# Kernel optimization log

Hardware: AMD Instinct MI355X
Metric: run time of the kernel (lower is better)

Reference implementation:

```python
import jax, jax.numpy as jnp
import numpy as np

N, E, B = 20000, 160000, 1024
MDIM, EDIM, H, L, PROP = 64, 16, 128, 4, 1000


def _lin(key, fan_in, fan_out, scale=None):
    s = scale if scale is not None else 1.0 / np.sqrt(fan_in)
    return (jax.random.normal(key, (fan_in, fan_out), jnp.float32) * s)


def setup_inputs() -> dict:
    key = jax.random.key(0)
    ks = iter(jax.random.split(key, 64))
    d = {}
    d["x"] = jax.random.normal(next(ks), (N, MDIM), jnp.float32)
    d["pos"] = jax.random.normal(next(ks), (N, 3), jnp.float32)
    d["edge_attr"] = jax.random.normal(next(ks), (E, EDIM), jnp.float32)
    d["edge_index"] = jax.random.randint(next(ks), (2, E), 0, N)
    d["batch"] = jnp.sort(jax.random.randint(next(ks), (N,), 0, B))
    # EGNN embeddings
    d["emb_in_w"] = _lin(next(ks), MDIM, H); d["emb_in_b"] = jnp.zeros((H,), jnp.float32)
    d["emb_out_w"] = _lin(next(ks), H, H); d["emb_out_b"] = jnp.zeros((H,), jnp.float32)
    # per-layer E_GCL params, stacked over layers
    ein = 2 * H + 1 + EDIM  # [h_row, h_col, radial, edge_attr]
    d["edge_w1"] = jnp.stack([_lin(next(ks), ein, H) for _ in range(L)]); d["edge_b1"] = jnp.zeros((L, H), jnp.float32)
    d["edge_w2"] = jnp.stack([_lin(next(ks), H, H) for _ in range(L)]); d["edge_b2"] = jnp.zeros((L, H), jnp.float32)
    d["node_w1"] = jnp.stack([_lin(next(ks), 2 * H, H) for _ in range(L)]); d["node_b1"] = jnp.zeros((L, H), jnp.float32)
    d["node_w2"] = jnp.stack([_lin(next(ks), H, H) for _ in range(L)]); d["node_b2"] = jnp.zeros((L, H), jnp.float32)
    d["coord_w1"] = jnp.stack([_lin(next(ks), H, H) for _ in range(L)]); d["coord_b1"] = jnp.zeros((L, H), jnp.float32)
    d["coord_w2"] = jnp.stack([_lin(next(ks), H, 1, scale=0.001) for _ in range(L)])  # xavier gain=0.001, no bias
    # end_layers: 2 ResBlocks (Dropout->Linear->SiLU->Linear) + head
    d["res_w1"] = jnp.stack([_lin(next(ks), H, H) for _ in range(2)]); d["res_b1"] = jnp.zeros((2, H), jnp.float32)
    d["res_w2"] = jnp.stack([_lin(next(ks), H, H) for _ in range(2)]); d["res_b2"] = jnp.zeros((2, H), jnp.float32)
    d["head_w"] = _lin(next(ks), H, PROP); d["head_b"] = jnp.zeros((PROP,), jnp.float32)
    return d


def _egnn_forward(x, pos, edge_attr, edge_index, batch,
                  emb_in_w, emb_in_b, emb_out_w, emb_out_b,
                  edge_w1, edge_b1, edge_w2, edge_b2,
                  node_w1, node_b1, node_w2, node_b2,
                  coord_w1, coord_b1, coord_w2,
                  res_w1, res_b1, res_w2, res_b2, head_w, head_b):
    silu = jax.nn.silu
    row, col = edge_index[0], edge_index[1]
    h = x @ emb_in_w + emb_in_b                                   # [N, H]
    # edge in-degree counts for coords_agg='mean' (clamped to >=1)
    cnt = jax.ops.segment_sum(jnp.ones((E, 1), h.dtype), row, num_segments=N)
    cnt = jnp.maximum(cnt, 1.0)
    for l in range(L):
        coord_diff = pos[row] - pos[col]                          # [E, 3]
        radial = jnp.sum(coord_diff * coord_diff, axis=-1, keepdims=True)  # [E, 1]
        # edge model
        e_in = jnp.concatenate([h[row], h[col], radial, edge_attr], axis=-1)
        m = silu(silu(e_in @ edge_w1[l] + edge_b1[l]) @ edge_w2[l] + edge_b2[l])  # [E, H]
        # coord model (coords_agg='mean')
        trans = coord_diff * (silu(m @ coord_w1[l] + coord_b1[l]) @ coord_w2[l])  # [E, 3]
        pos = pos + jax.ops.segment_sum(trans, row, num_segments=N) / cnt
        # node model (residual=True)
        agg = jax.ops.segment_sum(m, row, num_segments=N)         # [N, H]
        n_in = jnp.concatenate([h, agg], axis=-1)
        h = h + (silu(n_in @ node_w1[l] + node_b1[l]) @ node_w2[l] + node_b2[l])
    h = h @ emb_out_w + emb_out_b
    g = jax.ops.segment_max(h, batch, num_segments=B)             # [B, H]
    for r in range(2):
        g = g + (silu(g @ res_w1[r] + res_b1[r]) @ res_w2[r] + res_b2[r])
    return g @ head_w + head_b                                    # [B, PROP]


def reference(x, pos, edge_attr, edge_index, batch,
              emb_in_w, emb_in_b, emb_out_w, emb_out_b,
              edge_w1, edge_b1, edge_w2, edge_b2,
              node_w1, node_b1, node_w2, node_b2,
              coord_w1, coord_b1, coord_w2,
              res_w1, res_b1, res_w2, res_b2, head_w, head_b):
    return _egnn_forward(x, pos, edge_attr, edge_index, batch,
                         emb_in_w, emb_in_b, emb_out_w, emb_out_b,
                         edge_w1, edge_b1, edge_w2, edge_b2,
                         node_w1, node_b1, node_w2, node_b2,
                         coord_w1, coord_b1, coord_w2,
                         res_w1, res_b1, res_w2, res_b2, head_w, head_b)
```

## Files before the change

kernel.cpp:

```cpp
#include <hip/hip_runtime.h>
#include <hip/hip_bf16.h>

#define HD 128
#define PROP 1000
#define NPB  8

typedef float f32x4 __attribute__((ext_vector_type(4)));
typedef short s16x8 __attribute__((ext_vector_type(8)));

__device__ __forceinline__ float silu_f(float v) { return v / (1.0f + __expf(-v)); }

__device__ __forceinline__ unsigned short f2bf(float f) {
    union { __hip_bfloat16 h; unsigned short u; } v;
    v.h = __float2bfloat16(f);
    return v.u;
}
__device__ __forceinline__ unsigned pk2(float a, float b) {
    union { __hip_bfloat162 h; unsigned u; } v;
    v.h = __float22bfloat162_rn(make_float2(a, b));
    return v.u;
}
__device__ __forceinline__ float bf2f_lo(unsigned u) { return __uint_as_float(u << 16); }
__device__ __forceinline__ float bf2f_hi(unsigned u) { return __uint_as_float(u & 0xffff0000u); }
__device__ __forceinline__ float4 ld4(const float* p) { return *(const float4*)p; }
__device__ __forceinline__ unsigned enc_max(float f) {
    unsigned u = __float_as_uint(f);
    return (u & 0x80000000u) ? ~u : (u | 0x80000000u);
}


__global__ void counti_kernel(const int* __restrict__ ei, int* __restrict__ cnt, int E) {
    int e = blockIdx.x * 256 + threadIdx.x;
    if (e < E) atomicAdd(&cnt[ei[e]], 1);
}

__global__ __launch_bounds__(1024) void scan_blk(
    const int* __restrict__ cnt, int* __restrict__ excl, int* __restrict__ bsum, int N)
{
    __shared__ int wsum[16], wexc[17];
    const int t = threadIdx.x, lane = t & 63, wid = t >> 6;
    const int gid = blockIdx.x * 1024 + t;
    int v = (gid < N) ? cnt[gid] : 0;
    int incl = v;
    #pragma unroll
    for (int d = 1; d < 64; d <<= 1) {
        int x = __shfl_up(incl, d, 64);
        if (lane >= d) incl += x;
    }
    if (lane == 63) wsum[wid] = incl;
    __syncthreads();
    if (t == 0) {
        int a = 0;
        #pragma unroll
        for (int w2 = 0; w2 < 16; ++w2) { wexc[w2] = a; a += wsum[w2]; }
        wexc[16] = a;
    }
    __syncthreads();
    if (gid < N) excl[gid] = wexc[wid] + incl - v;
    if (t == 0) bsum[blockIdx.x] = wexc[16];
}
__global__ __launch_bounds__(64) void scan_top(int* __restrict__ bsum, int nb) {
    const int lane = threadIdx.x;
    int v = (lane < nb) ? bsum[lane] : 0;
    int incl = v;
    #pragma unroll
    for (int d = 1; d < 64; d <<= 1) {
        int x = __shfl_up(incl, d, 64);
        if (lane >= d) incl += x;
    }
    if (lane < nb) bsum[lane] = incl - v;
}
__global__ void scan_add(const int* __restrict__ excl, const int* __restrict__ bsum,
                         int* __restrict__ rp, int* __restrict__ wp, int N, int E) {
    int gid = blockIdx.x * 256 + threadIdx.x;
    if (gid < N) {
        int r = excl[gid] + bsum[gid >> 10];
        rp[gid] = r; wp[gid] = r;
    }
    if (gid == 0) rp[N] = E;
}

__global__ void scatter_kernel(const int* __restrict__ ei, int* __restrict__ wp,
                               int* __restrict__ perm, int* __restrict__ rows_s,
                               int* __restrict__ cols_s, int E) {
    int e = blockIdx.x * 256 + threadIdx.x;
    if (e < E) {
        int r = ei[e];
        int p = atomicAdd(&wp[r], 1);
        perm[p] = e;
        rows_s[p] = r;
        cols_s[p] = ei[E + e];
    }
}

__global__ void eattr_perm_kernel(const float* __restrict__ eattr, const int* __restrict__ perm,
                                  unsigned short* __restrict__ eperm, int E) {
    int i = blockIdx.x * 256 + threadIdx.x;
    if (i >= E) return;
    const float* src = eattr + (size_t)perm[i] * 16;
    float4 a = ld4(src), b = ld4(src + 4), c = ld4(src + 8), d = ld4(src + 12);
    unsigned short* dst = eperm + (size_t)i * 16;
    *(uint4*)dst       = make_uint4(pk2(a.x, a.y), pk2(a.z, a.w), pk2(b.x, b.y), pk2(b.z, b.w));
    *(uint4*)(dst + 8) = make_uint4(pk2(c.x, c.y), pk2(c.z, c.w), pk2(d.x, d.y), pk2(d.z, d.w));
}

__global__ void prep_w1nc(const float* __restrict__ ew1, unsigned short* __restrict__ dst) {
    int idx = blockIdx.x * 256 + threadIdx.x;
    if (idx >= 4 * 256 * 128) return;
    int k = idx & 127, o2 = (idx >> 7) & 255, l = idx >> 15;
    dst[idx] = f2bf(ew1[((size_t)l * 273 + k + ((o2 >> 7) << 7)) * 128 + (o2 & 127)]);
}
__global__ void prep_wattr(const float* __restrict__ ew1, unsigned short* __restrict__ dst) {
    int idx = blockIdx.x * 256 + threadIdx.x;
    if (idx >= 4 * 128 * 32) return;
    int k = idx & 31, o = (idx >> 5) & 127, l = idx >> 12;
    int ksrc = (k < 16) ? (257 + k) : (k == 16 ? 256 : -1);
    float v = (ksrc >= 0) ? ew1[((size_t)l * 273 + ksrc) * 128 + o] : 0.0f;
    dst[idx] = f2bf(v);
}
__global__ void prep_t(const float* __restrict__ src, unsigned short* __restrict__ dst, int K) {
    int idx = blockIdx.x * 256 + threadIdx.x;
    if (idx >= 4 * 128 * K) return;
    int k = idx % K, o = (idx / K) & 127, l = idx / (K * 128);
    dst[idx] = f2bf(src[((size_t)l * K + k) * 128 + o]);
}
__global__ void prep_t1(const float* __restrict__ src, unsigned short* __restrict__ dst) {
    int idx = blockIdx.x * 256 + threadIdx.x;
    if (idx >= 128 * 128) return;
    int k = idx & 127, o = idx >> 7;
    dst[idx] = f2bf(src[(size_t)k * 128 + o]);
}
__global__ void prep_t_sig(const float* __restrict__ src, unsigned short* __restrict__ dst) {
    int idx = blockIdx.x * 256 + threadIdx.x;
    if (idx >= 4 * 128 * 128) return;
    int k = idx & 127, o = (idx >> 7) & 127, l = idx >> 14;
    int ks = ((k >> 2) & 7) * 16 + ((k >> 5) << 2) + (k & 3);
    dst[idx] = f2bf(src[((size_t)l * 128 + ks) * 128 + o]);
}
__global__ void prep_wemb(const float* __restrict__ src, unsigned short* __restrict__ dst) {
    int idx = blockIdx.x * 256 + threadIdx.x;
    if (idx >= 128 * 64) return;
    int k = idx & 63, o = idx >> 6;
    dst[idx] = f2bf(src[(size_t)k * 128 + o]);
}

__global__ __launch_bounds__(128) void emb_pre_kernel(
    const float* __restrict__ x, const unsigned short* __restrict__ wembt,
    const float* __restrict__ bemb,
    const unsigned short* __restrict__ w1nc, const float* __restrict__ b1,
    float* __restrict__ h, unsigned short* __restrict__ apre, int N)
{
    __shared__ __align__(16) char s_xt[32 * 128];
    __shared__ __align__(16) char s_h[32 * 256];
    const int tid = threadIdx.x;
    const int lane = tid & 63, wid = tid >> 6;
    const int lr = lane & 15, kg = lane >> 4;
    const int n0 = blockIdx.x * 32 + wid * 16;
    {
        int n16 = lane >> 2, q = lane & 3;
        int nn = min(n0 + n16, N - 1);
        int sw2 = (n16 & 7) << 4;
        char* row = s_xt + (wid * 16 + n16) * 128;
        #pragma unroll
        for (int it = 0; it < 4; ++it) {
            float4 v = ld4(x + (size_t)nn * 64 + q * 16 + it * 4);
            *(uint2*)(row + ((q * 32 + it * 8) ^ sw2)) = make_uint2(pk2(v.x, v.y), pk2(v.z, v.w));
        }
    }
    const int nd = n0 + lr;
    const int sw = (lr & 7) << 4;
    f32x4 acc[8];
    #pragma unroll
    for (int mf = 0; mf < 8; ++mf) acc[mf] = (f32x4){0.f, 0.f, 0.f, 0.f};
    {
        const char* brow = s_xt + (wid * 16 + lr) * 128;
        for (int ks = 0; ks < 2; ++ks) {
            s16x8 b = *(const s16x8*)(brow + ((ks * 64 + kg * 16) ^ sw));
            #pragma unroll
            for (int mf = 0; mf < 8; ++mf) {
                s16x8 a = *(const s16x8*)(wembt + (size_t)(mf * 16 + lr) * 64 + ks * 32 + kg * 8);
                acc[mf] = __builtin_amdgcn_mfma_f32_16x16x32_bf16(a, b, acc[mf], 0, 0, 0);
            }
        }
    }
    char* hrow = s_h + (wid * 16 + lr) * 256;
    #pragma unroll
    for (int mf = 0; mf < 8; ++mf) {
        f32x4 bb = *(const f32x4*)(bemb + mf * 16 + kg * 4);
        float v0 = acc[mf][0] + bb[0];
        float v1 = acc[mf][1] + bb[1];
        float v2 = acc[mf][2] + bb[2];
        float v3 = acc[mf][3] + bb[3];
        if (nd < N) *(f32x4*)(h + (size_t)nd * HD + mf * 16 + kg * 4) = (f32x4){v0, v1, v2, v3};
        *(uint2*)(hrow + ((mf * 32 + kg * 8) ^ sw)) = make_uint2(pk2(v0, v1), pk2(v2, v3));
    }
    f32x4 acc2[16];
    #pragma unroll
    for (int mf = 0; mf < 16; ++mf) acc2[mf] = (f32x4){0.f, 0.f, 0.f, 0.f};
    for (int ks = 0; ks < 4; ++ks) {
        s16x8 b = *(const s16x8*)(hrow + ((ks * 64 + kg * 16) ^ sw));
        #pragma unroll
        for (int mf = 0; mf < 16; ++mf) {
            s16x8 a = *(const s16x8*)(w1nc + (size_t)(mf * 16 + lr) * 128 + ks * 32 + kg * 8);
            acc2[mf] = __builtin_amdgcn_mfma_f32_16x16x32_bf16(a, b, acc2[mf], 0, 0, 0);
        }
    }
    if (nd < N) {
        #pragma unroll
        for (int mf = 0; mf < 16; ++mf) {
            float b0 = 0.f, b1v = 0.f, b2v = 0.f, b3v = 0.f;
            if (mf < 8) {
                f32x4 bb = *(const f32x4*)(b1 + mf * 16 + kg * 4);
                b0 = bb[0]; b1v = bb[1]; b2v = bb[2]; b3v = bb[3];
            }
            int pos = ((mf >> 3) << 7) + kg * 32 + (mf & 7) * 4;
            *(uint2*)(apre + (size_t)nd * 256 + pos) =
                make_uint2(pk2(acc2[mf][0] + b0, acc2[mf][1] + b1v), pk2(acc2[mf][2] + b2v, acc2[mf][3] + b3v));
        }
    }
}

__global__ __launch_bounds__(64) void edge_compute_kernel(
    const float* __restrict__ pos, const unsigned short* __restrict__ apre,
    const unsigned short* __restrict__ eperm,
    const int* __restrict__ rows_s, const int* __restrict__ cols_s,
    const unsigned short* __restrict__ wattr,
    const unsigned short* __restrict__ wt2, const float* __restrict__ b2,
    const unsigned short* __restrict__ cwt1, const float* __restrict__ cb1,
    const float* __restrict__ cw2,
    unsigned short* __restrict__ medge, float* __restrict__ trans, int E)
{
    __shared__ __align__(16) char s_m[16 * 256];
    __shared__ __align__(16) char s_g[16 * 256];

    int wg = blockIdx.x;
    {
        int nper = gridDim.x >> 3;
        if ((gridDim.x & 7) == 0) wg = (wg & 7) * nper + (wg >> 3);
    }
    const int lane = threadIdx.x;
    const int lr = lane & 15, kg = lane >> 4;
    const int i0 = wg * 16;
    const int i = i0 + lr;
    const bool valid = i < E;
    const int ic = min(i, E - 1);
    const int r = rows_s[ic], c = cols_s[ic];

    {
        int e = lane >> 2, q = lane & 3;
        int ce = cols_s[min(i0 + e, E - 1)];
        const char* src = (const char*)(apre + (size_t)ce * 256 + 128);
        char* dst = s_g + e * 256;
        int sw2 = (e & 7) << 4;
        #pragma unroll
        for (int it = 0; it < 4; ++it) {
            uint4 v = *(const uint4*)(src + it * 64 + q * 16);
            *(uint4*)(dst + ((it * 64 + q * 16) ^ sw2)) = v;
        }
    }

    float dx = pos[r*3+0] - pos[c*3+0];
    float dy = pos[r*3+1] - pos[c*3+1];
    float dz = pos[r*3+2] - pos[c*3+2];
    float rad = dx*dx + dy*dy + dz*dz;

    union { s16x8 v; unsigned u[4]; } battr;
    if (kg < 2) {
        battr.v = *(const s16x8*)(eperm + (size_t)ic * 16 + kg * 8);
    } else {
        battr.u[0] = (kg == 2) ? pk2(rad, 0.f) : 0u;
        battr.u[1] = 0u; battr.u[2] = 0u; battr.u[3] = 0u;
    }

    uint4 rgq[4];
    {
        const unsigned short* rb = apre + (size_t)r * 256 + kg * 32;
        #pragma unroll
        for (int q = 0; q < 4; ++q) rgq[q] = *(const uint4*)(rb + q * 8);
    }
    uint4 cgq[4];
    {
        const char* g = s_g + lr * 256;
        int swl = (lr & 7) << 4;
        #pragma unroll
        for (int q = 0; q < 4; ++q)
            cgq[q] = *(const uint4*)(g + ((kg * 64 + q * 16) ^ swl));
    }

    char* mrow = s_m + lr * 256;
    const int sw = (lr & 7) << 4;

    f32x4 acc[8];
    #pragma unroll
    for (int mf = 0; mf < 8; ++mf) acc[mf] = (f32x4){0.f, 0.f, 0.f, 0.f};
    #pragma unroll
    for (int mf = 0; mf < 8; ++mf) {
        s16x8 a = *(const s16x8*)(wattr + (size_t)(mf * 16 + lr) * 32 + kg * 8);
        acc[mf] = __builtin_amdgcn_mfma_f32_16x16x32_bf16(a, battr.v, acc[mf], 0, 0, 0);
    }
    #pragma unroll
    for (int mf = 0; mf < 8; ++mf) {
        unsigned rlo = ((const unsigned*)&rgq[mf >> 1])[(mf & 1) * 2];
        unsigned rhi = ((const unsigned*)&rgq[mf >> 1])[(mf & 1) * 2 + 1];
        unsigned clo = ((const unsigned*)&cgq[mf >> 1])[(mf & 1) * 2];
        unsigned chi = ((const unsigned*)&cgq[mf >> 1])[(mf & 1) * 2 + 1];
        float v0 = silu_f(acc[mf][0] + bf2f_lo(rlo) + bf2f_lo(clo));
        float v1 = silu_f(acc[mf][1] + bf2f_hi(rlo) + bf2f_hi(clo));
        float v2 = silu_f(acc[mf][2] + bf2f_lo(rhi) + bf2f_lo(chi));
        float v3 = silu_f(acc[mf][3] + bf2f_hi(rhi) + bf2f_hi(chi));
        *(uint2*)(mrow + ((kg * 64 + mf * 8) ^ sw)) = make_uint2(pk2(v0, v1), pk2(v2, v3));
    }

    #pragma unroll
    for (int mf = 0; mf < 8; ++mf) acc[mf] = (f32x4){0.f, 0.f, 0.f, 0.f};
    for (int ks = 0; ks < 4; ++ks) {
        s16x8 b = *(const s16x8*)(mrow + ((ks * 64 + kg * 16) ^ sw));
        #pragma unroll
        for (int mf = 0; mf < 8; ++mf) {
            s16x8 a = *(const s16x8*)(wt2 + (size_t)(mf * 16 + lr) * 128 + ks * 32 + kg * 8);
            acc[mf] = __builtin_amdgcn_mfma_f32_16x16x32_bf16(a, b, acc[mf], 0, 0, 0);
        }
    }
    #pragma unroll
    for (int mf = 0; mf < 8; ++mf) {
        f32x4 bb = *(const f32x4*)(b2 + mf * 16 + kg * 4);
        float v0 = silu_f(acc[mf][0] + bb[0]);
        float v1 = silu_f(acc[mf][1] + bb[1]);
        float v2 = silu_f(acc[mf][2] + bb[2]);
        float v3 = silu_f(acc[mf][3] + bb[3]);
        *(uint2*)(mrow + ((mf * 32 + kg * 8) ^ sw)) = make_uint2(pk2(v0, v1), pk2(v2, v3));
    }

    #pragma unroll
    for (int mf = 0; mf < 8; ++mf) acc[mf] = (f32x4){0.f, 0.f, 0.f, 0.f};
    for (int ks = 0; ks < 4; ++ks) {
        s16x8 b = *(const s16x8*)(mrow + ((ks * 64 + kg * 16) ^ sw));
        #pragma unroll
        for (int mf = 0; mf < 8; ++mf) {
            s16x8 a = *(const s16x8*)(cwt1 + (size_t)(mf * 16 + lr) * 128 + ks * 32 + kg * 8);
            acc[mf] = __builtin_amdgcn_mfma_f32_16x16x32_bf16(a, b, acc[mf], 0, 0, 0);
        }
    }

    {
        int e = lane >> 2, q = lane & 3;
        int ie = i0 + e;
        if (ie < E) {
            const char* src = s_m + e * 256;
            int sw2 = (e & 7) << 4;
            char* dst = (char*)(medge + (size_t)ie * HD);
            #pragma unroll
            for (int it = 0; it < 4; ++it) {
                uint4 v = *(const uint4*)(src + ((it * 64 + q * 16) ^ sw2));
                *(uint4*)(dst + it * 64 + q * 16) = v;
            }
        }
    }

    float part = 0.f;
    #pragma unroll
    for (int mf = 0; mf < 8; ++mf) {
        f32x4 bb = *(const f32x4*)(cb1 + mf * 16 + kg * 4);
        f32x4 cw = *(const f32x4*)(cw2 + mf * 16 + kg * 4);
        part += silu_f(acc[mf][0] + bb[0]) * cw[0];
        part += silu_f(acc[mf][1] + bb[1]) * cw[1];
        part += silu_f(acc[mf][2] + bb[2]) * cw[2];
        part += silu_f(acc[mf][3] + bb[3]) * cw[3];
    }
    part += __shfl_xor(part, 16, 64);
    part += __shfl_xor(part, 32, 64);
    if (valid && kg == 0)
        *(float4*)(trans + (size_t)i * 4) = make_float4(dx * part, dy * part, dz * part, 0.f);
}

__global__ __launch_bounds__(64) void node_fused_kernel(
    float* __restrict__ h, const unsigned short* __restrict__ medge,
    const float* __restrict__ trans, const int* __restrict__ rp,
    float* __restrict__ pos,
    const unsigned short* __restrict__ nw1t, const float* __restrict__ nb1,
    const unsigned short* __restrict__ nw2t, const float* __restrict__ nb2,
    const unsigned short* __restrict__ w1nc_next, const float* __restrict__ b1_next,
    unsigned short* __restrict__ apre, int N, int has_next)
{
    __shared__ __align__(16) char s_x[16 * 512];
    const int lane = threadIdx.x;
    const int lr = lane & 15, kg = lane >> 4;
    const int n0 = blockIdx.x * 16;
    {
        int n16 = lane >> 2, q = lane & 3;
        int nn = min(n0 + n16, N - 1);
        int sw2 = (n16 & 7) << 4;
        char* row = s_x + n16 * 512;
        #pragma unroll
        for (int it = 0; it < 8; ++it) {
            int c2 = q * 32 + it * 4;
            float4 v = ld4(h + (size_t)nn * HD + c2);
            *(uint2*)(row + ((c2 * 2) ^ sw2)) = make_uint2(pk2(v.x, v.y), pk2(v.z, v.w));
        }
        const int s = rp[nn], e2 = rp[nn + 1];
        float a[32];
        #pragma unroll
        for (int t = 0; t < 32; ++t) a[t] = 0.f;
        for (int j = s; j < e2; ++j) {
            const unsigned short* mp = medge + (size_t)j * HD + q * 32;
            #pragma unroll
            for (int v4 = 0; v4 < 4; ++v4) {
                uint4 w = *(const uint4*)(mp + v4 * 8);
                a[v4*8+0] += bf2f_lo(w.x); a[v4*8+1] += bf2f_hi(w.x);
                a[v4*8+2] += bf2f_lo(w.y); a[v4*8+3] += bf2f_hi(w.y);
                a[v4*8+4] += bf2f_lo(w.z); a[v4*8+5] += bf2f_hi(w.z);
                a[v4*8+6] += bf2f_lo(w.w); a[v4*8+7] += bf2f_hi(w.w);
            }
        }
        #pragma unroll
        for (int it2 = 0; it2 < 4; ++it2) {
            uint4 w = make_uint4(pk2(a[it2*8+0], a[it2*8+1]), pk2(a[it2*8+2], a[it2*8+3]),
                                 pk2(a[it2*8+4], a[it2*8+5]), pk2(a[it2*8+6], a[it2*8+7]));
            *(uint4*)(row + ((256 + q * 64 + it2 * 16) ^ sw2)) = w;
        }
        if (q < 3 && n0 + n16 < N) {
            float pa = 0.f;
            for (int j = s; j < e2; ++j) pa += trans[(size_t)j * 4 + q];
            pos[(size_t)(n0 + n16) * 3 + q] += pa / fmaxf((float)(e2 - s), 1.0f);
        }
    }
    const int nd = n0 + lr;
    char* brow = s_x + lr * 512;
    const int sw = (lr & 7) << 4;
    f32x4 acc[8];
    #pragma unroll
    for (int mf = 0; mf < 8; ++mf) acc[mf] = (f32x4){0.f, 0.f, 0.f, 0.f};
    for (int ks = 0; ks < 8; ++ks) {
        s16x8 b = *(const s16x8*)(brow + ((ks * 64 + kg * 16) ^ sw));
        #pragma unroll
        for (int mf = 0; mf < 8; ++mf) {
            s16x8 a = *(const s16x8*)(nw1t + (size_t)(mf * 16 + lr) * 256 + ks * 32 + kg * 8);
            acc[mf] = __builtin_amdgcn_mfma_f32_16x16x32_bf16(a, b, acc[mf], 0, 0, 0);
        }
    }
    #pragma unroll
    for (int mf = 0; mf < 8; ++mf) {
        f32x4 bb = *(const f32x4*)(nb1 + mf * 16 + kg * 4);
        float v0 = silu_f(acc[mf][0] + bb[0]);
        float v1 = silu_f(acc[mf][1] + bb[1]);
        float v2 = silu_f(acc[mf][2] + bb[2]);
        float v3 = silu_f(acc[mf][3] + bb[3]);
        *(uint2*)(brow + ((mf * 32 + kg * 8) ^ sw)) = make_uint2(pk2(v0, v1), pk2(v2, v3));
    }
    #pragma unroll
    for (int mf = 0; mf < 8; ++mf) acc[mf] = (f32x4){0.f, 0.f, 0.f, 0.f};
    for (int ks = 0; ks < 4; ++ks) {
        s16x8 b = *(const s16x8*)(brow + ((ks * 64 + kg * 16) ^ sw));
        #pragma unroll
        for (int mf = 0; mf < 8; ++mf) {
            s16x8 a = *(const s16x8*)(nw2t + (size_t)(mf * 16 + lr) * 128 + ks * 32 + kg * 8);
            acc[mf] = __builtin_amdgcn_mfma_f32_16x16x32_bf16(a, b, acc[mf], 0, 0, 0);
        }
    }
    uint2 hpk[8];
    if (nd < N) {
        #pragma unroll
        for (int mf = 0; mf < 8; ++mf) {
            f32x4 bb = *(const f32x4*)(nb2 + mf * 16 + kg * 4);
            float* hp = h + (size_t)nd * HD + mf * 16 + kg * 4;
            f32x4 hv = *(const f32x4*)hp;
            hv[0] += acc[mf][0] + bb[0];
            hv[1] += acc[mf][1] + bb[1];
            hv[2] += acc[mf][2] + bb[2];
            hv[3] += acc[mf][3] + bb[3];
            *(f32x4*)hp = hv;
            hpk[mf] = make_uint2(pk2(hv[0], hv[1]), pk2(hv[2], hv[3]));
        }
    }
    if (!has_next) return;
    #pragma unroll
    for (int mf = 0; mf < 8; ++mf)
        *(uint2*)(brow + ((mf * 32 + kg * 8) ^ sw)) = hpk[mf];
    f32x4 acc2[16];
    #pragma unroll
    for (int mf = 0; mf < 16; ++mf) acc2[mf] = (f32x4){0.f, 0.f, 0.f, 0.f};
    for (int ks = 0; ks < 4; ++ks) {
        s16x8 b = *(const s16x8*)(brow + ((ks * 64 + kg * 16) ^ sw));
        #pragma unroll
        for (int mf = 0; mf < 16; ++mf) {
            s16x8 a = *(const s16x8*)(w1nc_next + (size_t)(mf * 16 + lr) * 128 + ks * 32 + kg * 8);
            acc2[mf] = __builtin_amdgcn_mfma_f32_16x16x32_bf16(a, b, acc2[mf], 0, 0, 0);
        }
    }
    if (nd < N) {
        #pragma unroll
        for (int mf = 0; mf < 16; ++mf) {
            float b0 = 0.f, b1v = 0.f, b2v = 0.f, b3v = 0.f;
            if (mf < 8) {
                f32x4 bb = *(const f32x4*)(b1_next + mf * 16 + kg * 4);
                b0 = bb[0]; b1v = bb[1]; b2v = bb[2]; b3v = bb[3];
            }
            int pos2 = ((mf >> 3) << 7) + kg * 32 + (mf & 7) * 4;
            *(uint2*)(apre + (size_t)nd * 256 + pos2) =
                make_uint2(pk2(acc2[mf][0] + b0, acc2[mf][1] + b1v), pk2(acc2[mf][2] + b2v, acc2[mf][3] + b3v));
        }
    }
}

__global__ void ginit_kernel(unsigned* __restrict__ g_enc, int n) {
    int i = blockIdx.x * 256 + threadIdx.x;
    if (i < n) g_enc[i] = 0x007FFFFFu;
}

__global__ __launch_bounds__(64) void embout_mfma_kernel(
    const float* __restrict__ h, const unsigned short* __restrict__ wot,
    const float* __restrict__ b, const int* __restrict__ batch,
    unsigned* __restrict__ g_enc, int N)
{
    __shared__ __align__(16) char s_h[16 * 256];
    __shared__ __align__(16) float s_out[16 * 128];
    const int lane = threadIdx.x;
    const int lr = lane & 15, kg = lane >> 4;
    const int n0 = blockIdx.x * 16;
    {
        int n16 = lane >> 2, q = lane & 3;
        int nn = min(n0 + n16, N - 1);
        int sw2 = (n16 & 7) << 4;
        char* row = s_h + n16 * 256;
        #pragma unroll
        for (int it = 0; it < 8; ++it) {
            int c2 = q * 32 + it * 4;
            float4 v = ld4(h + (size_t)nn * HD + c2);
            *(uint2*)(row + ((c2 * 2) ^ sw2)) = make_uint2(pk2(v.x, v.y), pk2(v.z, v.w));
        }
    }
    const char* brow = s_h + lr * 256;
    const int sw = (lr & 7) << 4;
    f32x4 acc[8];
    #pragma unroll
    for (int mf = 0; mf < 8; ++mf) acc[mf] = (f32x4){0.f, 0.f, 0.f, 0.f};
    for (int ks = 0; ks < 4; ++ks) {
        s16x8 bv = *(const s16x8*)(brow + ((ks * 64 + kg * 16) ^ sw));
        #pragma unroll
        for (int mf = 0; mf < 8; ++mf) {
            s16x8 a = *(const s16x8*)(wot + (size_t)(mf * 16 + lr) * 128 + ks * 32 + kg * 8);
            acc[mf] = __builtin_amdgcn_mfma_f32_16x16x32_bf16(a, bv, acc[mf], 0, 0, 0);
        }
    }
    #pragma unroll
    for (int mf = 0; mf < 8; ++mf) {
        f32x4 bb = *(const f32x4*)(b + mf * 16 + kg * 4);
        f32x4 v = { acc[mf][0] + bb[0], acc[mf][1] + bb[1], acc[mf][2] + bb[2], acc[mf][3] + bb[3] };
        *(f32x4*)(s_out + lr * 128 + mf * 16 + kg * 4) = v;
    }
    const int nmax = min(16, N - n0);
    float m0 = -3.4e38f, m1 = -3.4e38f;
    int cur = batch[n0];
    for (int e = 0; e < nmax; ++e) {
        int bi = batch[n0 + e];
        if (bi != cur) {
            atomicMax(&g_enc[(size_t)cur * HD + lane], enc_max(m0));
            atomicMax(&g_enc[(size_t)cur * HD + 64 + lane], enc_max(m1));
            m0 = -3.4e38f; m1 = -3.4e38f; cur = bi;
        }
        m0 = fmaxf(m0, s_out[e * 128 + lane]);
        m1 = fmaxf(m1, s_out[e * 128 + 64 + lane]);
    }
    atomicMax(&g_enc[(size_t)cur * HD + lane], enc_max(m0));
    atomicMax(&g_enc[(size_t)cur * HD + 64 + lane], enc_max(m1));
}

__global__ __launch_bounds__(128) void resblock_kernel(
    const unsigned* __restrict__ g_enc,
    const float* __restrict__ rw1, const float* __restrict__ rb1,
    const float* __restrict__ rw2, const float* __restrict__ rb2,
    float* __restrict__ g)
{
    __shared__ float s_g[HD];
    __shared__ float s_t[HD];
    const int b = blockIdx.x, j = threadIdx.x;
    unsigned u = g_enc[(size_t)b * HD + j];
    float v = (u & 0x80000000u) ? __uint_as_float(u & 0x7FFFFFFFu) : __uint_as_float(~u);
    s_g[j] = v;
    __syncthreads();
    for (int r = 0; r < 2; ++r) {
        float a1 = rb1[r * HD + j];
        for (int k = 0; k < HD; ++k) a1 += s_g[k] * rw1[(size_t)r * HD * HD + (size_t)k * HD + j];
        s_t[j] = silu_f(a1);
        __syncthreads();
        float a2 = rb2[r * HD + j];
        for (int k = 0; k < HD; ++k) a2 += s_t[k] * rw2[(size_t)r * HD * HD + (size_t)k * HD + j];
        __syncthreads();
        s_g[j] += a2;
        __syncthreads();
    }
    g[(size_t)b * HD + j] = s_g[j];
}

__global__ __launch_bounds__(256) void head_kernel(
    const float* __restrict__ g, const float* __restrict__ hw, const float* __restrict__ hb,
    float* __restrict__ out, int B)
{
    __shared__ __align__(16) float s_g[HD][8];
    const int b0 = blockIdx.y * 8;
    const int p = blockIdx.x * 256 + threadIdx.x;
    for (int t = threadIdx.x; t < 8 * HD; t += 256) {
        int b = t & 7, k = t >> 3;
        s_g[k][b] = g[(size_t)min(b0 + b, B - 1) * HD + k];
    }
    __syncthreads();
    if (p >= PROP) return;
    float hbp = hb[p];
    float acc[8];
    #pragma unroll
    for (int b = 0; b < 8; ++b) acc[b] = hbp;
    for (int k = 0; k < HD; ++k) {
        float w = hw[(size_t)k * PROP + p];
        float4 g0 = *(const float4*)&s_g[k][0];
        float4 g1 = *(const float4*)&s_g[k][4];
        acc[0] += g0.x * w; acc[1] += g0.y * w; acc[2] += g0.z * w; acc[3] += g0.w * w;
        acc[4] += g1.x * w; acc[5] += g1.y * w; acc[6] += g1.z * w; acc[7] += g1.w * w;
    }
    #pragma unroll
    for (int b = 0; b < 8; ++b)
        if (b0 + b < B) out[(size_t)(b0 + b) * PROP + p] = acc[b];
}

extern "C" void kernel_launch(void* const* d_in, const int* in_sizes, int n_in,
                              void* d_out, int out_size, void* d_ws, size_t ws_size,
                              hipStream_t stream)
{
    const float* x        = (const float*)d_in[0];
    const float* pos_in   = (const float*)d_in[1];
    const float* eattr    = (const float*)d_in[2];
    const int*   ei       = (const int*)d_in[3];
    const int*   batch    = (const int*)d_in[4];
    const float* emb_in_w = (const float*)d_in[5];
    const float* emb_in_b = (const float*)d_in[6];
    const float* emb_out_w= (const float*)d_in[7];
    const float* emb_out_b= (const float*)d_in[8];
    const float* ew1 = (const float*)d_in[9];
    const float* eb1 = (const float*)d_in[10];
    const float* ew2 = (const float*)d_in[11];
    const float* eb2 = (const float*)d_in[12];
    const float* nw1 = (const float*)d_in[13];
    const float* nb1 = (const float*)d_in[14];
    const float* nw2 = (const float*)d_in[15];
    const float* nb2 = (const float*)d_in[16];
    const float* cw1 = (const float*)d_in[17];
    const float* cb1 = (const float*)d_in[18];
    const float* cw2 = (const float*)d_in[19];
    const float* rw1 = (const float*)d_in[20];
    const float* rb1 = (const float*)d_in[21];
    const float* rw2 = (const float*)d_in[22];
    const float* rb2 = (const float*)d_in[23];
    const float* hw  = (const float*)d_in[24];
    const float* hb  = (const float*)d_in[25];
    float* out = (float*)d_out;
    (void)ws_size;

    const int N = in_sizes[0] / 64;
    const int E = in_sizes[2] / 16;
    const int B = out_size / PROP;

    float* wsf = (float*)d_ws;
    float* pos_cur = wsf;   wsf += (size_t)N * 3;
    float* h       = wsf;   wsf += (size_t)N * HD;
    float* g       = wsf;   wsf += (size_t)B * HD;
    float* trans   = wsf;   wsf += (size_t)E * 4;
    wsf += (4 - (((size_t)(wsf - (float*)d_ws)) & 3)) & 3;
    unsigned short* apre  = (unsigned short*)wsf;
    unsigned short* eperm = apre  + (size_t)N * 256;
    unsigned short* w1nc  = eperm + (size_t)E * 16;
    unsigned short* wattr = w1nc  + (size_t)4 * 256 * 128;
    unsigned short* wt2   = wattr + (size_t)4 * 128 * 32;
    unsigned short* cwt1  = wt2   + (size_t)4 * 128 * 128;
    unsigned short* nw1t  = cwt1  + (size_t)4 * 128 * 128;
    unsigned short* nw2t  = nw1t  + (size_t)4 * 128 * 256;
    unsigned short* wembt = nw2t  + (size_t)4 * 128 * 128;
    unsigned short* wot   = wembt + (size_t)128 * 64;
    unsigned short* medge = wot   + (size_t)128 * 128;
    int* ip   = (int*)(medge + (size_t)E * HD);
    unsigned* g_enc = (unsigned*)ip;  ip += (size_t)B * HD;
    int* cnt_i = ip;  ip += N;
    int* rp    = ip;  ip += N + 1;
    int* wp    = ip;  ip += N;
    int* excl  = ip;  ip += N;
    int* bsum  = ip;  ip += 64;
    int* perm  = ip;  ip += E;
    int* rows_s= ip;  ip += E;
    int* cols_s= ip;  ip += E;

    prep_w1nc<<<(4 * 256 * 128 + 255) / 256, 256, 0, stream>>>(ew1, w1nc);
    prep_wattr<<<(4 * 128 * 32 + 255) / 256, 256, 0, stream>>>(ew1, wattr);
    prep_t_sig<<<(4 * 128 * 128 + 255) / 256, 256, 0, stream>>>(ew2, wt2);
    prep_t<<<(4 * 128 * 128 + 255) / 256, 256, 0, stream>>>(cw1, cwt1, 128);
    prep_t<<<(4 * 128 * 256 + 255) / 256, 256, 0, stream>>>(nw1, nw1t, 256);
    prep_t<<<(4 * 128 * 128 + 255) / 256, 256, 0, stream>>>(nw2, nw2t, 128);
    prep_wemb<<<(128 * 64 + 255) / 256, 256, 0, stream>>>(emb_in_w, wembt);
    prep_t1<<<(128 * 128 + 255) / 256, 256, 0, stream>>>(emb_out_w, wot);

    hipMemsetAsync(cnt_i, 0, (size_t)N * sizeof(int), stream);
    counti_kernel<<<(E + 255) / 256, 256, 0, stream>>>(ei, cnt_i, E);
    const int nb = (N + 1023) / 1024;
    scan_blk<<<nb, 1024, 0, stream>>>(cnt_i, excl, bsum, N);
    scan_top<<<1, 64, 0, stream>>>(bsum, nb);
    scan_add<<<(N + 255) / 256, 256, 0, stream>>>(excl, bsum, rp, wp, N, E);
    scatter_kernel<<<(E + 255) / 256, 256, 0, stream>>>(ei, wp, perm, rows_s, cols_s, E);
    eattr_perm_kernel<<<(E + 255) / 256, 256, 0, stream>>>(eattr, perm, eperm, E);

    hipMemcpyAsync(pos_cur, pos_in, (size_t)N * 3 * sizeof(float),
                   hipMemcpyDeviceToDevice, stream);

    emb_pre_kernel<<<(N + 31) / 32, 128, 0, stream>>>(x, wembt, emb_in_b, w1nc, eb1, h, apre, N);
    const int nblk = (N + 15) / 16;
    for (int l = 0; l < 4; ++l) {
        edge_compute_kernel<<<(E + 15) / 16, 64, 0, stream>>>(
            pos_cur, apre, eperm, rows_s, cols_s,
            wattr + (size_t)l * 128 * 32,
            wt2  + (size_t)l * 128 * 128, eb2 + (size_t)l * HD,
            cwt1 + (size_t)l * 128 * 128, cb1 + (size_t)l * HD,
            cw2 + (size_t)l * HD,
            medge, trans, E);
        node_fused_kernel<<<nblk, 64, 0, stream>>>(
            h, medge, trans, rp, pos_cur,
            nw1t + (size_t)l * 128 * 256, nb1 + (size_t)l * HD,
            nw2t + (size_t)l * 128 * 128, nb2 + (size_t)l * HD,
            w1nc + (size_t)(l + 1 < 4 ? l + 1 : 0) * 256 * 128,
            eb1 + (size_t)(l + 1 < 4 ? l + 1 : 0) * HD,
            apre, N, l < 3 ? 1 : 0);
    }

    ginit_kernel<<<(B * HD + 255) / 256, 256, 0, stream>>>(g_enc, B * HD);
    embout_mfma_kernel<<<nblk, 64, 0, stream>>>(h, wot, emb_out_b, batch, g_enc, N);
    resblock_kernel<<<B, 128, 0, stream>>>(g_enc, rw1, rb1, rw2, rb2, g);
    head_kernel<<<dim3((PROP + 255) / 256, (B + 7) / 8), 256, 0, stream>>>(g, hw, hb, out, B);
}
```

Measured before the change: 662.7 us.

## Process two 16-edge tiles per wave in edge kernel and merge prep launches

The edge compute kernel now handles 32 edges per 64-thread workgroup as two 16-edge tiles. Each weight fragment loaded from global memory feeds two MFMAs, one per tile, which halves weight-load traffic per edge and gives the scheduler more independent work. In exchange the kernel uses twice the accumulator registers and LDS, which may lower occupancy. Separately, the eight weight-prep kernels and the g_enc init kernel are folded into one prep_all launch to cut launch overhead.

```diff
diff --git a/kernel.cpp b/kernel.cpp
--- a/kernel.cpp
+++ b/kernel.cpp
@@ -104,44 +104,69 @@
     *(uint4*)(dst + 8) = make_uint4(pk2(c.x, c.y), pk2(c.z, c.w), pk2(d.x, d.y), pk2(d.z, d.w));
 }
 
-__global__ void prep_w1nc(const float* __restrict__ ew1, unsigned short* __restrict__ dst) {
+__global__ void prep_all(
+    const float* __restrict__ ew1, const float* __restrict__ ew2, const float* __restrict__ cw1,
+    const float* __restrict__ nw1, const float* __restrict__ nw2,
+    const float* __restrict__ emb_in_w, const float* __restrict__ emb_out_w,
+    unsigned short* __restrict__ w1nc, unsigned short* __restrict__ wattr,
+    unsigned short* __restrict__ wt2, unsigned short* __restrict__ cwt1,
+    unsigned short* __restrict__ nw1t, unsigned short* __restrict__ nw2t,
+    unsigned short* __restrict__ wembt, unsigned short* __restrict__ wot,
+    unsigned* __restrict__ g_enc, int ng)
+{
     int idx = blockIdx.x * 256 + threadIdx.x;
-    if (idx >= 4 * 256 * 128) return;
-    int k = idx & 127, o2 = (idx >> 7) & 255, l = idx >> 15;
-    dst[idx] = f2bf(ew1[((size_t)l * 273 + k + ((o2 >> 7) << 7)) * 128 + (o2 & 127)]);
-}
-__global__ void prep_wattr(const float* __restrict__ ew1, unsigned short* __restrict__ dst) {
-    int idx = blockIdx.x * 256 + threadIdx.x;
-    if (idx >= 4 * 128 * 32) return;
-    int k = idx & 31, o = (idx >> 5) & 127, l = idx >> 12;
-    int ksrc = (k < 16) ? (257 + k) : (k == 16 ? 256 : -1);
-    float v = (ksrc >= 0) ? ew1[((size_t)l * 273 + ksrc) * 128 + o] : 0.0f;
-    dst[idx] = f2bf(v);
-}
-__global__ void prep_t(const float* __restrict__ src, unsigned short* __restrict__ dst, int K) {
-    int idx = blockIdx.x * 256 + threadIdx.x;
-    if (idx >= 4 * 128 * K) return;
-    int k = idx % K, o = (idx / K) & 127, l = idx / (K * 128);
-    dst[idx] = f2bf(src[((size_t)l * K + k) * 128 + o]);
-}
-__global__ void prep_t1(const float* __restrict__ src, unsigned short* __restrict__ dst) {
-    int idx = blockIdx.x * 256 + threadIdx.x;
-    if (idx >= 128 * 128) return;
-    int k = idx & 127, o = idx >> 7;
-    dst[idx] = f2bf(src[(size_t)k * 128 + o]);
-}
-__global__ void prep_t_sig(const float* __restrict__ src, unsigned short* __restrict__ dst) {
-    int idx = blockIdx.x * 256 + threadIdx.x;
-    if (idx >= 4 * 128 * 128) return;
-    int k = idx & 127, o = (idx >> 7) & 127, l = idx >> 14;
-    int ks = ((k >> 2) & 7) * 16 + ((k >> 5) << 2) + (k & 3);
-    dst[idx] = f2bf(src[((size_t)l * 128 + ks) * 128 + o]);
-}
-__global__ void prep_wemb(const float* __restrict__ src, unsigned short* __restrict__ dst) {
-    int idx = blockIdx.x * 256 + threadIdx.x;
-    if (idx >= 128 * 64) return;
-    int k = idx & 63, o = idx >> 6;
-    dst[idx] = f2bf(src[(size_t)k * 128 + o]);
+    if (idx < 131072) {
+        int k = idx & 127, o2 = (idx >> 7) & 255, l = idx >> 15;
+        w1nc[idx] = f2bf(ew1[((size_t)l * 273 + k + ((o2 >> 7) << 7)) * 128 + (o2 & 127)]);
+        return;
+    }
+    idx -= 131072;
+    if (idx < 16384) {
+        int k = idx & 31, o = (idx >> 5) & 127, l = idx >> 12;
+        int ksrc = (k < 16) ? (257 + k) : (k == 16 ? 256 : -1);
+        float v = (ksrc >= 0) ? ew1[((size_t)l * 273 + ksrc) * 128 + o] : 0.0f;
+        wattr[idx] = f2bf(v);
+        return;
+    }
+    idx -= 16384;
+    if (idx < 65536) {
+        int k = idx & 127, o = (idx >> 7) & 127, l = idx >> 14;
+        int ks = ((k >> 2) & 7) * 16 + ((k >> 5) << 2) + (k & 3);
+        wt2[idx] = f2bf(ew2[((size_t)l * 128 + ks) * 128 + o]);
+        return;
+    }
+    idx -= 65536;
+    if (idx < 65536) {
+        int k = idx & 127, o = (idx >> 7) & 127, l = idx >> 14;
+        cwt1[idx] = f2bf(cw1[((size_t)l * 128 + k) * 128 + o]);
+        return;
+    }
+    idx -= 65536;
+    if (idx < 131072) {
+        int k = idx % 256, o = (idx / 256) & 127, l = idx / (256 * 128);
+        nw1t[idx] = f2bf(nw1[((size_t)l * 256 + k) * 128 + o]);
+        return;
+    }
+    idx -= 131072;
+    if (idx < 65536) {
+        int k = idx & 127, o = (idx >> 7) & 127, l = idx >> 14;
+        nw2t[idx] = f2bf(nw2[((size_t)l * 128 + k) * 128 + o]);
+        return;
+    }
+    idx -= 65536;
+    if (idx < 8192) {
+        int k = idx & 63, o = idx >> 6;
+        wembt[idx] = f2bf(emb_in_w[(size_t)k * 128 + o]);
+        return;
+    }
+    idx -= 8192;
+    if (idx < 16384) {
+        int k = idx & 127, o = idx >> 7;
+        wot[idx] = f2bf(emb_out_w[(size_t)k * 128 + o]);
+        return;
+    }
+    idx -= 16384;
+    if (idx < ng) g_enc[idx] = 0x007FFFFFu;
 }
 
 __global__ __launch_bounds__(128) void emb_pre_kernel(
@@ -230,8 +255,8 @@
     const float* __restrict__ cw2,
     unsigned short* __restrict__ medge, float* __restrict__ trans, int E)
 {
-    __shared__ __align__(16) char s_m[16 * 256];
-    __shared__ __align__(16) char s_g[16 * 256];
+    __shared__ __align__(16) char s_m[2][16 * 256];
+    __shared__ __align__(16) char s_g[2][16 * 256];
 
     int wg = blockIdx.x;
     {
@@ -240,137 +265,173 @@
     }
     const int lane = threadIdx.x;
     const int lr = lane & 15, kg = lane >> 4;
-    const int i0 = wg * 16;
-    const int i = i0 + lr;
-    const bool valid = i < E;
-    const int ic = min(i, E - 1);
-    const int r = rows_s[ic], c = cols_s[ic];
+    const int i0 = wg * 32;
+    const int iA = i0 + lr, iB = i0 + 16 + lr;
+    const bool vA = iA < E, vB = iB < E;
+    const int icA = min(iA, E - 1), icB = min(iB, E - 1);
+    const int rA = rows_s[icA], cA = cols_s[icA];
+    const int rB = rows_s[icB], cB = cols_s[icB];
 
     {
         int e = lane >> 2, q = lane & 3;
-        int ce = cols_s[min(i0 + e, E - 1)];
-        const char* src = (const char*)(apre + (size_t)ce * 256 + 128);
-        char* dst = s_g + e * 256;
         int sw2 = (e & 7) << 4;
         #pragma unroll
-        for (int it = 0; it < 4; ++it) {
-            uint4 v = *(const uint4*)(src + it * 64 + q * 16);
-            *(uint4*)(dst + ((it * 64 + q * 16) ^ sw2)) = v;
-        }
-    }
-
-    float dx = pos[r*3+0] - pos[c*3+0];
-    float dy = pos[r*3+1] - pos[c*3+1];
-    float dz = pos[r*3+2] - pos[c*3+2];
-    float rad = dx*dx + dy*dy + dz*dz;
-
-    union { s16x8 v; unsigned u[4]; } battr;
+        for (int t = 0; t < 2; ++t) {
+            int ce = cols_s[min(i0 + t * 16 + e, E - 1)];
+            const char* src = (const char*)(apre + (size_t)ce * 256 + 128);
+            char* dst = s_g[t] + e * 256;
+            #pragma unroll
+            for (int it = 0; it < 4; ++it) {
+                uint4 v = *(const uint4*)(src + it * 64 + q * 16);
+                *(uint4*)(dst + ((it * 64 + q * 16) ^ sw2)) = v;
+            }
+        }
+    }
+
+    float dxA = pos[rA*3+0] - pos[cA*3+0];
+    float dyA = pos[rA*3+1] - pos[cA*3+1];
+    float dzA = pos[rA*3+2] - pos[cA*3+2];
+    float dxB = pos[rB*3+0] - pos[cB*3+0];
+    float dyB = pos[rB*3+1] - pos[cB*3+1];
+    float dzB = pos[rB*3+2] - pos[cB*3+2];
+    float radA = dxA*dxA + dyA*dyA + dzA*dzA;
+    float radB = dxB*dxB + dyB*dyB + dzB*dzB;
+
+    union { s16x8 v; unsigned u[4]; } battrA, battrB;
     if (kg < 2) {
-        battr.v = *(const s16x8*)(eperm + (size_t)ic * 16 + kg * 8);
+        battrA.v = *(const s16x8*)(eperm + (size_t)icA * 16 + kg * 8);
+        battrB.v = *(const s16x8*)(eperm + (size_t)icB * 16 + kg * 8);
     } else {
-        battr.u[0] = (kg == 2) ? pk2(rad, 0.f) : 0u;
-        battr.u[1] = 0u; battr.u[2] = 0u; battr.u[3] = 0u;
-    }
-
-    uint4 rgq[4];
-    {
-        const unsigned short* rb = apre + (size_t)r * 256 + kg * 32;
-        #pragma unroll
-        for (int q = 0; q < 4; ++q) rgq[q] = *(const uint4*)(rb + q * 8);
-    }
-    uint4 cgq[4];
-    {
-        const char* g = s_g + lr * 256;
-        int swl = (lr & 7) << 4;
-        #pragma unroll
-        for (int q = 0; q < 4; ++q)
-            cgq[q] = *(const uint4*)(g + ((kg * 64 + q * 16) ^ swl));
-    }
-
-    char* mrow = s_m + lr * 256;
+        battrA.u[0] = (kg == 2) ? pk2(radA, 0.f) : 0u;
+        battrA.u[1] = 0u; battrA.u[2] = 0u; battrA.u[3] = 0u;
+        battrB.u[0] = (kg == 2) ? pk2(radB, 0.f) : 0u;
+        battrB.u[1] = 0u; battrB.u[2] = 0u; battrB.u[3] = 0u;
+    }
+
+    char* mrowA = s_m[0] + lr * 256;
+    char* mrowB = s_m[1] + lr * 256;
     const int sw = (lr & 7) << 4;
 
-    f32x4 acc[8];
-    #pragma unroll
-    for (int mf = 0; mf < 8; ++mf) acc[mf] = (f32x4){0.f, 0.f, 0.f, 0.f};
+    f32x4 aA[8], aB[8];
+    #pragma unroll
+    for (int mf = 0; mf < 8; ++mf) { aA[mf] = (f32x4){0,0,0,0}; aB[mf] = (f32x4){0,0,0,0}; }
+
     #pragma unroll
     for (int mf = 0; mf < 8; ++mf) {
         s16x8 a = *(const s16x8*)(wattr + (size_t)(mf * 16 + lr) * 32 + kg * 8);
-        acc[mf] = __builtin_amdgcn_mfma_f32_16x16x32_bf16(a, battr.v, acc[mf], 0, 0, 0);
-    }
-    #pragma unroll
-    for (int mf = 0; mf < 8; ++mf) {
-        unsigned rlo = ((const unsigned*)&rgq[mf >> 1])[(mf & 1) * 2];
-        unsigned rhi = ((const unsigned*)&rgq[mf >> 1])[(mf & 1) * 2 + 1];
-        unsigned clo = ((const unsigned*)&cgq[mf >> 1])[(mf & 1) * 2];
-        unsigned chi = ((const unsigned*)&cgq[mf >> 1])[(mf & 1) * 2 + 1];
-        float v0 = silu_f(acc[mf][0] + bf2f_lo(rlo) + bf2f_lo(clo));
-        float v1 = silu_f(acc[mf][1] + bf2f_hi(rlo) + bf2f_hi(clo));
-        float v2 = silu_f(acc[mf][2] + bf2f_lo(rhi) + bf2f_lo(chi));
-        float v3 = silu_f(acc[mf][3] + bf2f_hi(rhi) + bf2f_hi(chi));
-        *(uint2*)(mrow + ((kg * 64 + mf * 8) ^ sw)) = make_uint2(pk2(v0, v1), pk2(v2, v3));
-    }
-
-    #pragma unroll
-    for (int mf = 0; mf < 8; ++mf) acc[mf] = (f32x4){0.f, 0.f, 0.f, 0.f};
+        aA[mf] = __builtin_amdgcn_mfma_f32_16x16x32_bf16(a, battrA.v, aA[mf], 0, 0, 0);
+        aB[mf] = __builtin_amdgcn_mfma_f32_16x16x32_bf16(a, battrB.v, aB[mf], 0, 0, 0);
+    }
+    #pragma unroll
+    for (int t = 0; t < 2; ++t) {
+        const int r = t ? rB : rA;
+        f32x4* acc = t ? aB : aA;
+        char* mrow = t ? mrowB : mrowA;
+        uint4 rgq[4], cgq[4];
+        {
+            const unsigned short* rb = apre + (size_t)r * 256 + kg * 32;
+            const char* g = s_g[t] + lr * 256;
+            #pragma unroll
+            for (int q = 0; q < 4; ++q) {
+                rgq[q] = *(const uint4*)(rb + q * 8);
+                cgq[q] = *(const uint4*)(g + ((kg * 64 + q * 16) ^ sw));
+            }
+        }
+        #pragma unroll
+        for (int mf = 0; mf < 8; ++mf) {
+            unsigned rlo = ((const unsigned*)&rgq[mf >> 1])[(mf & 1) * 2];
+            unsigned rhi = ((const unsigned*)&rgq[mf >> 1])[(mf & 1) * 2 + 1];
+            unsigned clo = ((const unsigned*)&cgq[mf >> 1])[(mf & 1) * 2];
+            unsigned chi = ((const unsigned*)&cgq[mf >> 1])[(mf & 1) * 2 + 1];
+            float v0 = silu_f(acc[mf][0] + bf2f_lo(rlo) + bf2f_lo(clo));
+            float v1 = silu_f(acc[mf][1] + bf2f_hi(rlo) + bf2f_hi(clo));
+            float v2 = silu_f(acc[mf][2] + bf2f_lo(rhi) + bf2f_lo(chi));
+            float v3 = silu_f(acc[mf][3] + bf2f_hi(rhi) + bf2f_hi(chi));
+            *(uint2*)(mrow + ((kg * 64 + mf * 8) ^ sw)) = make_uint2(pk2(v0, v1), pk2(v2, v3));
+        }
+    }
+
+    #pragma unroll
+    for (int mf = 0; mf < 8; ++mf) { aA[mf] = (f32x4){0,0,0,0}; aB[mf] = (f32x4){0,0,0,0}; }
     for (int ks = 0; ks < 4; ++ks) {
-        s16x8 b = *(const s16x8*)(mrow + ((ks * 64 + kg * 16) ^ sw));
+        s16x8 bA = *(const s16x8*)(mrowA + ((ks * 64 + kg * 16) ^ sw));
+        s16x8 bB = *(const s16x8*)(mrowB + ((ks * 64 + kg * 16) ^ sw));
         #pragma unroll
         for (int mf = 0; mf < 8; ++mf) {
             s16x8 a = *(const s16x8*)(wt2 + (size_t)(mf * 16 + lr) * 128 + ks * 32 + kg * 8);
-            acc[mf] = __builtin_amdgcn_mfma_f32_16x16x32_bf16(a, b, acc[mf], 0, 0, 0);
-        }
-    }
-    #pragma unroll
-    for (int mf = 0; mf < 8; ++mf) {
-        f32x4 bb = *(const f32x4*)(b2 + mf * 16 + kg * 4);
-        float v0 = silu_f(acc[mf][0] + bb[0]);
-        float v1 = silu_f(acc[mf][1] + bb[1]);
-        float v2 = silu_f(acc[mf][2] + bb[2]);
-        float v3 = silu_f(acc[mf][3] + bb[3]);
-        *(uint2*)(mrow + ((mf * 32 + kg * 8) ^ sw)) = make_uint2(pk2(v0, v1), pk2(v2, v3));
-    }
-
-    #pragma unroll
-    for (int mf = 0; mf < 8; ++mf) acc[mf] = (f32x4){0.f, 0.f, 0.f, 0.f};
+            aA[mf] = __builtin_amdgcn_mfma_f32_16x16x32_bf16(a, bA, aA[mf], 0, 0, 0);
+            aB[mf] = __builtin_amdgcn_mfma_f32_16x16x32_bf16(a, bB, aB[mf], 0, 0, 0);
+        }
+    }
+    #pragma unroll
+    for (int t = 0; t < 2; ++t) {
+        f32x4* acc = t ? aB : aA;
+        char* mrow = t ? mrowB : mrowA;
+        #pragma unroll
+        for (int mf = 0; mf < 8; ++mf) {
+            f32x4 bb = *(const f32x4*)(b2 + mf * 16 + kg * 4);
+            float v0 = silu_f(acc[mf][0] + bb[0]);
+            float v1 = silu_f(acc[mf][1] + bb[1]);
+            float v2 = silu_f(acc[mf][2] + bb[2]);
+            float v3 = silu_f(acc[mf][3] + bb[3]);
+            *(uint2*)(mrow + ((mf * 32 + kg * 8) ^ sw)) = make_uint2(pk2(v0, v1), pk2(v2, v3));
+        }
+    }
+
+    #pragma unroll
+    for (int mf = 0; mf < 8; ++mf) { aA[mf] = (f32x4){0,0,0,0}; aB[mf] = (f32x4){0,0,0,0}; }
     for (int ks = 0; ks < 4; ++ks) {
-        s16x8 b = *(const s16x8*)(mrow + ((ks * 64 + kg * 16) ^ sw));
+        s16x8 bA = *(const s16x8*)(mrowA + ((ks * 64 + kg * 16) ^ sw));
+        s16x8 bB = *(const s16x8*)(mrowB + ((ks * 64 + kg * 16) ^ sw));
         #pragma unroll
         for (int mf = 0; mf < 8; ++mf) {
             s16x8 a = *(const s16x8*)(cwt1 + (size_t)(mf * 16 + lr) * 128 + ks * 32 + kg * 8);
-            acc[mf] = __builtin_amdgcn_mfma_f32_16x16x32_bf16(a, b, acc[mf], 0, 0, 0);
+            aA[mf] = __builtin_amdgcn_mfma_f32_16x16x32_bf16(a, bA, aA[mf], 0, 0, 0);
+            aB[mf] = __builtin_amdgcn_mfma_f32_16x16x32_bf16(a, bB, aB[mf], 0, 0, 0);
         }
     }
 
     {
         int e = lane >> 2, q = lane & 3;
-        int ie = i0 + e;
-        if (ie < E) {
-            const char* src = s_m + e * 256;
-            int sw2 = (e & 7) << 4;
-            char* dst = (char*)(medge + (size_t)ie * HD);
-            #pragma unroll
-            for (int it = 0; it < 4; ++it) {
-                uint4 v = *(const uint4*)(src + ((it * 64 + q * 16) ^ sw2));
-                *(uint4*)(dst + it * 64 + q * 16) = v;
+        int sw2 = (e & 7) << 4;
+        #pragma unroll
+        for (int t = 0; t < 2; ++t) {
+            int ie = i0 + t * 16 + e;
+            if (ie < E) {
+                const char* src = s_m[t] + e * 256;
+                char* dst = (char*)(medge + (size_t)ie * HD);
+                #pragma unroll
+                for (int it = 0; it < 4; ++it) {
+                    uint4 v = *(const uint4*)(src + ((it * 64 + q * 16) ^ sw2));
+                    *(uint4*)(dst + it * 64 + q * 16) = v;
+                }
             }
         }
     }
 
-    float part = 0.f;
-    #pragma unroll
-    for (int mf = 0; mf < 8; ++mf) {
-        f32x4 bb = *(const f32x4*)(cb1 + mf * 16 + kg * 4);
-        f32x4 cw = *(const f32x4*)(cw2 + mf * 16 + kg * 4);
-        part += silu_f(acc[mf][0] + bb[0]) * cw[0];
-        part += silu_f(acc[mf][1] + bb[1]) * cw[1];
-        part += silu_f(acc[mf][2] + bb[2]) * cw[2];
-        part += silu_f(acc[mf][3] + bb[3]) * cw[3];
-    }
-    part += __shfl_xor(part, 16, 64);
-    part += __shfl_xor(part, 32, 64);
-    if (valid && kg == 0)
-        *(float4*)(trans + (size_t)i * 4) = make_float4(dx * part, dy * part, dz * part, 0.f);
+    #pragma unroll
+    for (int t = 0; t < 2; ++t) {
+        f32x4* acc = t ? aB : aA;
+        float part = 0.f;
+        #pragma unroll
+        for (int mf = 0; mf < 8; ++mf) {
+            f32x4 bb = *(const f32x4*)(cb1 + mf * 16 + kg * 4);
+            f32x4 cw = *(const f32x4*)(cw2 + mf * 16 + kg * 4);
+            part += silu_f(acc[mf][0] + bb[0]) * cw[0];
+            part += silu_f(acc[mf][1] + bb[1]) * cw[1];
+            part += silu_f(acc[mf][2] + bb[2]) * cw[2];
+            part += silu_f(acc[mf][3] + bb[3]) * cw[3];
+        }
+        part += __shfl_xor(part, 16, 64);
+        part += __shfl_xor(part, 32, 64);
+        if (kg == 0) {
+            int ie = i0 + t * 16 + lr;
+            if (ie < E) {
+                float dx = t ? dxB : dxA, dy = t ? dyB : dyA, dz = t ? dzB : dzA;
+                *(float4*)(trans + (size_t)ie * 4) = make_float4(dx * part, dy * part, dz * part, 0.f);
+            }
+        }
+    }
 }
 
 __global__ __launch_bounds__(64) void node_fused_kernel(
@@ -500,11 +561,6 @@
                 make_uint2(pk2(acc2[mf][0] + b0, acc2[mf][1] + b1v), pk2(acc2[mf][2] + b2v, acc2[mf][3] + b3v));
         }
     }
-}
-
-__global__ void ginit_kernel(unsigned* __restrict__ g_enc, int n) {
-    int i = blockIdx.x * 256 + threadIdx.x;
-    if (i < n) g_enc[i] = 0x007FFFFFu;
 }
 
 __global__ __launch_bounds__(64) void embout_mfma_kernel(
@@ -686,14 +742,11 @@
     int* rows_s= ip;  ip += E;
     int* cols_s= ip;  ip += E;
 
-    prep_w1nc<<<(4 * 256 * 128 + 255) / 256, 256, 0, stream>>>(ew1, w1nc);
-    prep_wattr<<<(4 * 128 * 32 + 255) / 256, 256, 0, stream>>>(ew1, wattr);
-    prep_t_sig<<<(4 * 128 * 128 + 255) / 256, 256, 0, stream>>>(ew2, wt2);
-    prep_t<<<(4 * 128 * 128 + 255) / 256, 256, 0, stream>>>(cw1, cwt1, 128);
-    prep_t<<<(4 * 128 * 256 + 255) / 256, 256, 0, stream>>>(nw1, nw1t, 256);
-    prep_t<<<(4 * 128 * 128 + 255) / 256, 256, 0, stream>>>(nw2, nw2t, 128);
-    prep_wemb<<<(128 * 64 + 255) / 256, 256, 0, stream>>>(emb_in_w, wembt);
-    prep_t1<<<(128 * 128 + 255) / 256, 256, 0, stream>>>(emb_out_w, wot);
+    const int ng = B * HD;
+    const int prep_total = 131072 + 16384 + 65536 + 65536 + 131072 + 65536 + 8192 + 16384 + ng;
+    prep_all<<<(prep_total + 255) / 256, 256, 0, stream>>>(
+        ew1, ew2, cw1, nw1, nw2, emb_in_w, emb_out_w,
+        w1nc, wattr, wt2, cwt1, nw1t, nw2t, wembt, wot, g_enc, ng);
 
     hipMemsetAsync(cnt_i, 0, (size_t)N * sizeof(int), stream);
     counti_kernel<<<(E + 255) / 256, 256, 0, stream>>>(ei, cnt_i, E);
@@ -710,7 +763,7 @@
     emb_pre_kernel<<<(N + 31) / 32, 128, 0, stream>>>(x, wembt, emb_in_b, w1nc, eb1, h, apre, N);
     const int nblk = (N + 15) / 16;
     for (int l = 0; l < 4; ++l) {
-        edge_compute_kernel<<<(E + 15) / 16, 64, 0, stream>>>(
+        edge_compute_kernel<<<(E + 31) / 32, 64, 0, stream>>>(
             pos_cur, apre, eperm, rows_s, cols_s,
             wattr + (size_t)l * 128 * 32,
             wt2  + (size_t)l * 128 * 128, eb2 + (size_t)l * HD,
@@ -726,7 +779,6 @@
             apre, N, l < 3 ? 1 : 0);
     }
 
-    ginit_kernel<<<(B * HD + 255) / 256, 256, 0, stream>>>(g_enc, B * HD);
     embout_mfma_kernel<<<nblk, 64, 0, stream>>>(h, wot, emb_out_b, batch, g_enc, N);
     resblock_kernel<<<B, 128, 0, stream>>>(g_enc, rw1, rb1, rw2, rb2, g);
     head_kernel<<<dim3((PROP + 255) / 256, (B + 7) / 8), 256, 0, stream>>>(g, hw, hb, out, B);
```

After: 604.0 us. 8.9% less time.
